# Optimization experiments

Hardware: AMD Instinct MI355X
Metric: run time of the kernel (lower is better)

The kernel has to match this reference:

```python
import jax, jax.numpy as jnp
import numpy as np
import math

HEAD_N = 8
IN_FEATS = 512
BATCH, LENG = 4, 2048
LN_EPS = 1e-5


def setup_inputs() -> dict:
    key = jax.random.key(0)
    ks = jax.random.split(key, 16)
    d = IN_FEATS
    inp = {
        "q": jax.random.normal(ks[0], (BATCH, LENG, d), jnp.float32),
        "k": jax.random.normal(ks[1], (BATCH, LENG, d), jnp.float32),
        "v": jax.random.normal(ks[2], (BATCH, LENG, d), jnp.float32),
        # 4 Linear(in_feats, in_feats): weights [out,in] torch-style, bias [out]
        "Wq": jax.random.normal(ks[3], (d, d), jnp.float32) * 0.02,
        "bq": jnp.zeros((d,), jnp.float32),
        "Wk": jax.random.normal(ks[4], (d, d), jnp.float32) * 0.02,
        "bk": jnp.zeros((d,), jnp.float32),
        "Wv": jax.random.normal(ks[5], (d, d), jnp.float32) * 0.02,
        "bv": jnp.zeros((d,), jnp.float32),
        "Wo": jax.random.normal(ks[6], (d, d), jnp.float32) * 0.02,
        "bo": jnp.zeros((d,), jnp.float32),
        "gamma": jnp.ones((d,), jnp.float32),
        "beta": jnp.zeros((d,), jnp.float32),
    }
    return inp


def _split_heads(x, W, b):
    # Linear then reshape exactly as the torch code: (B,L,D)->(B,L,H,dh)->(B,H,L,dh)->(B*H,L,dh)
    B, L, D = x.shape
    dh = D // HEAD_N
    y = x @ W.T + b
    y = y.reshape(B, L, HEAD_N, dh).transpose(0, 2, 1, 3).reshape(B * HEAD_N, L, dh)
    return y


def reference(q, k, v, Wq, bq, Wk, bk, Wv, bv, Wo, bo, gamma, beta):
    residual = q
    B, L, D = q.shape
    dh = D // HEAD_N
    qh = _split_heads(q, Wq, bq)  # [B*H, L, dh]
    kh = _split_heads(k, Wk, bk)
    vh = _split_heads(v, Wv, bv)

    scores = jnp.einsum("nqd,nkd->nqk", qh, kh) / math.sqrt(dh)  # [B*H, L, L]
    raw_att = jax.nn.softmax(scores, axis=-1)
    att = jnp.einsum("nqk,nkd->nqd", raw_att, vh)  # [B*H, L, dh]

    # Faithful to the original (buggy) merge: reshape (B*H,L,dh) AS IF layout were (H,B,L,dh)
    att = att.reshape(HEAD_N, B, L, dh).transpose(1, 2, 0, 3).reshape(B, L, D)

    att = att @ Wo.T + bo
    # dropout is identity in eval/reference mode
    x = att + residual
    mu = jnp.mean(x, axis=-1, keepdims=True)
    var = jnp.mean(jnp.square(x - mu), axis=-1, keepdims=True)
    out = (x - mu) / jnp.sqrt(var + LN_EPS) * gamma + beta
    return (out, raw_att)
```

## Files before the change

kernel.cpp:

```cpp
#include <hip/hip_runtime.h>
#include <hip/hip_bf16.h>

#define D_MODEL 512
#define SEQ 2048
#define NB 4
#define NH 8
#define DH 64
#define NHEADS 32
#define MROWS 8192

typedef __bf16 bf16_t;
typedef __bf16 bf16x4_t __attribute__((ext_vector_type(4)));
typedef __bf16 bf16x8_t __attribute__((ext_vector_type(8)));
typedef float f32x4_t __attribute__((ext_vector_type(4)));

__device__ inline f32x4_t mfma16(bf16x8_t a, bf16x8_t b, f32x4_t c) {
    return __builtin_amdgcn_mfma_f32_16x16x32_bf16(a, b, c, 0, 0, 0);
}

__global__ __launch_bounds__(256) void qkv_proj_all_kernel(
    const float* __restrict__ qp, const float* __restrict__ kp, const float* __restrict__ vp,
    const float* __restrict__ Wq, const float* __restrict__ bq,
    const float* __restrict__ Wk, const float* __restrict__ bk,
    const float* __restrict__ Wv, const float* __restrict__ bv,
    bf16_t* __restrict__ qfrag, bf16_t* __restrict__ kfrag, bf16_t* __restrict__ vfrag)
{
    __shared__ bf16_t As[128][72];
    __shared__ bf16_t Bs[128][72];

    const int mode = blockIdx.z;
    const float* X    = (mode == 0) ? qp : (mode == 1) ? kp : vp;
    const float* W    = (mode == 0) ? Wq : (mode == 1) ? Wk : Wv;
    const float* bias = (mode == 0) ? bq : (mode == 1) ? bk : bv;
    bf16_t* dst       = (mode == 0) ? qfrag : (mode == 1) ? kfrag : vfrag;

    const int t = threadIdx.x;
    const int lane = t & 63, w = t >> 6;
    const int lr = lane & 15, lg = lane >> 4;
    const int wm = w >> 1, wn = w & 1;
    const int m0 = blockIdx.x * 128, n0 = blockIdx.y * 128;

    f32x4_t acc[4][4];
#pragma unroll
    for (int i = 0; i < 4; i++)
#pragma unroll
        for (int j = 0; j < 4; j++) acc[i][j] = f32x4_t{0.f, 0.f, 0.f, 0.f};

    const int srow = t >> 4;
    const int scol = (t & 15) * 4;

    bf16_t (*Pa)[72] = (mode == 2) ? As : Bs;
    bf16_t (*Pb)[72] = (mode == 2) ? Bs : As;

    for (int kt = 0; kt < 8; kt++) {
        __syncthreads();
#pragma unroll
        for (int p = 0; p < 8; p++) {
            int row = p * 16 + srow;
            float4 va = *(const float4*)(X + (size_t)(m0 + row) * 512 + kt * 64 + scol);
            bf16x4_t ha = { (bf16_t)va.x, (bf16_t)va.y, (bf16_t)va.z, (bf16_t)va.w };
            *(bf16x4_t*)(&As[row][scol]) = ha;
            float4 vb = *(const float4*)(W + (size_t)(n0 + row) * 512 + kt * 64 + scol);
            bf16x4_t hb = { (bf16_t)vb.x, (bf16_t)vb.y, (bf16_t)vb.z, (bf16_t)vb.w };
            *(bf16x4_t*)(&Bs[row][scol]) = hb;
        }
        __syncthreads();
#pragma unroll
        for (int kk = 0; kk < 64; kk += 32) {
            bf16x8_t fa[4], fb[4];
#pragma unroll
            for (int i = 0; i < 4; i++)
                fa[i] = *(const bf16x8_t*)(&Pa[wm * 64 + i * 16 + lr][kk + lg * 8]);
#pragma unroll
            for (int j = 0; j < 4; j++)
                fb[j] = *(const bf16x8_t*)(&Pb[wn * 64 + j * 16 + lr][kk + lg * 8]);
#pragma unroll
            for (int i = 0; i < 4; i++)
#pragma unroll
                for (int j = 0; j < 4; j++)
                    acc[i][j] = mfma16(fa[i], fb[j], acc[i][j]);
        }
    }

    if (mode == 2) {
#pragma unroll
        for (int j = 0; j < 4; j++) {
            int col = n0 + wn * 64 + j * 16 + lr;
            float bval = bias[col];
            int h = col >> 6, d = col & 63;
#pragma unroll
            for (int i = 0; i < 4; i++) {
                int rbase = m0 + wm * 64 + i * 16 + lg * 4;
                int b = rbase >> 11, l0 = rbase & 2047;
                int win = l0 >> 5, kkg = l0 & 31;
                int pos0 = (kkg < 16) ? ((kkg >> 2) * 8) : (((kkg - 16) >> 2) * 8 + 4);
                bf16x4_t hv;
#pragma unroll
                for (int r = 0; r < 4; r++) hv[r] = (bf16_t)(acc[i][j][r] + bval);
                *(bf16x4_t*)(dst + ((((size_t)(b * NH + h) * 64 + win) * 64 + d) * 32 + pos0)) = hv;
            }
        }
    } else {
#pragma unroll
        for (int i = 0; i < 4; i++) {
            int featbase = n0 + wm * 64 + i * 16 + lg * 4;
            float4 b4 = *(const float4*)(bias + featbase);
            float bb[4] = { b4.x, b4.y, b4.z, b4.w };
            int h = featbase >> 6, d0 = featbase & 63;
            int c = (d0 & 31) >> 3, e0 = d0 & 7, fd = (d0 >= 32) ? 1 : 0;
#pragma unroll
            for (int j = 0; j < 4; j++) {
                int seq = m0 + wn * 64 + j * 16 + lr;
                int b = seq >> 11, l = seq & 2047;
                bf16x4_t hv;
#pragma unroll
                for (int r = 0; r < 4; r++) hv[r] = (bf16_t)(acc[i][j][r] + bb[r]);
                size_t idx;
                if (mode == 0) {
                    int qw = l >> 4, lp = (l & 15) + 16 * c;
                    idx = ((((size_t)(b * NH + h) * 128 + qw) * 2 + fd) * 64 + lp) * 8 + e0;
                } else {
                    int win = l >> 5, fk = (((l & 31) >= 16) ? 2 : 0) + fd;
                    int lp = (l & 15) + 16 * c;
                    idx = ((((size_t)(b * NH + h) * 64 + win) * 4 + fk) * 64 + lp) * 8 + e0;
                }
                *(bf16x4_t*)(dst + idx) = hv;
            }
        }
    }
}

__global__ __launch_bounds__(256, 2) void attn_kernel(
    const bf16_t* __restrict__ qfrag, const bf16_t* __restrict__ kfrag,
    const bf16_t* __restrict__ vfrag, float* __restrict__ probs,
    bf16_t* __restrict__ attw)
{
    __shared__ float stage[4][16][132];

    const int bh = blockIdx.y;
    const int t = threadIdx.x;
    const int lane = t & 63, w = t >> 6;
    const int lr = lane & 15, lg = lane >> 4;
    const int q0c0 = blockIdx.x * 128 + w * 32;
    const int q0c1 = q0c0 + 16;
    const int qw0 = q0c0 >> 4;

    const bf16_t* qfb = qfrag + (size_t)bh * 131072;
    const bf16x8_t qA0 = *(const bf16x8_t*)(qfb + ((size_t)(qw0 * 2 + 0) * 64 + lane) * 8);
    const bf16x8_t qA1 = *(const bf16x8_t*)(qfb + ((size_t)(qw0 * 2 + 1) * 64 + lane) * 8);
    const bf16x8_t qB0 = *(const bf16x8_t*)(qfb + ((size_t)(qw0 * 2 + 2) * 64 + lane) * 8);
    const bf16x8_t qB1 = *(const bf16x8_t*)(qfb + ((size_t)(qw0 * 2 + 3) * 64 + lane) * 8);

    const bf16_t* kfb = kfrag + (size_t)bh * 131072;
    const bf16_t* vfb = vfrag + (size_t)bh * 131072;

    float sum0 = 0.f;
    {
        const bf16_t* kp0 = kfb + lane * 8;
        bf16x8_t k00 = *(const bf16x8_t*)(kp0);
        bf16x8_t k01 = *(const bf16x8_t*)(kp0 + 512);
        bf16x8_t k10 = *(const bf16x8_t*)(kp0 + 1024);
        bf16x8_t k11 = *(const bf16x8_t*)(kp0 + 1536);
#pragma unroll 2
        for (int win = 0; win < 64; win++) {
            bf16x8_t n00 = k00, n01 = k01, n10 = k10, n11 = k11;
            if (win < 63) {
                const bf16_t* kp = kfb + (size_t)(win + 1) * 2048 + lane * 8;
                n00 = *(const bf16x8_t*)(kp);
                n01 = *(const bf16x8_t*)(kp + 512);
                n10 = *(const bf16x8_t*)(kp + 1024);
                n11 = *(const bf16x8_t*)(kp + 1536);
            }
            f32x4_t s0 = {0.f, 0.f, 0.f, 0.f}, s1 = {0.f, 0.f, 0.f, 0.f};
            s0 = mfma16(k00, qA0, s0);
            s0 = mfma16(k01, qA1, s0);
            s1 = mfma16(k10, qA0, s1);
            s1 = mfma16(k11, qA1, s1);
#pragma unroll
            for (int r = 0; r < 4; r++)
                sum0 += __expf(s0[r] * 0.125f) + __expf(s1[r] * 0.125f);
            k00 = n00; k01 = n01; k10 = n10; k11 = n11;
        }
    }
    sum0 += __shfl_xor(sum0, 16, 64);
    sum0 += __shfl_xor(sum0, 32, 64);
    const float ri0 = 1.0f / sum0;

    f32x4_t oacc[4];
#pragma unroll
    for (int db = 0; db < 4; db++) oacc[db] = f32x4_t{0.f, 0.f, 0.f, 0.f};
    float sum1 = 0.f;
    {
        float* pb = probs + (size_t)bh * SEQ * SEQ + (size_t)q0c0 * SEQ;
        const bf16_t* kp0 = kfb + lane * 8;
        bf16x8_t k00 = *(const bf16x8_t*)(kp0);
        bf16x8_t k01 = *(const bf16x8_t*)(kp0 + 512);
        bf16x8_t k10 = *(const bf16x8_t*)(kp0 + 1024);
        bf16x8_t k11 = *(const bf16x8_t*)(kp0 + 1536);

        for (int sw = 0; sw < 16; sw++) {
#pragma unroll
            for (int c = 0; c < 4; c++) {
                const int win = sw * 4 + c;
                bf16x8_t av[4];
#pragma unroll
                for (int db = 0; db < 4; db++)
                    av[db] = *(const bf16x8_t*)(vfb + (((size_t)win * 64 + db * 16 + lr) * 32 + lg * 8));
                bf16x8_t n00 = k00, n01 = k01, n10 = k10, n11 = k11;
                if (win < 63) {
                    const bf16_t* kp = kfb + (size_t)(win + 1) * 2048 + lane * 8;
                    n00 = *(const bf16x8_t*)(kp);
                    n01 = *(const bf16x8_t*)(kp + 512);
                    n10 = *(const bf16x8_t*)(kp + 1024);
                    n11 = *(const bf16x8_t*)(kp + 1536);
                }
                f32x4_t s0 = {0.f, 0.f, 0.f, 0.f}, s1 = {0.f, 0.f, 0.f, 0.f};
                s0 = mfma16(k00, qA0, s0);
                s0 = mfma16(k01, qA1, s0);
                s1 = mfma16(k10, qA0, s1);
                s1 = mfma16(k11, qA1, s1);
                float pl[8];
#pragma unroll
                for (int r = 0; r < 4; r++) {
                    pl[r]     = __expf(s0[r] * 0.125f) * ri0;
                    pl[4 + r] = __expf(s1[r] * 0.125f) * ri0;
                }
                const int c0_ = c * 32;
                f32x4_t lo = { pl[0], pl[1], pl[2], pl[3] };
                f32x4_t hi = { pl[4], pl[5], pl[6], pl[7] };
                *(f32x4_t*)(&stage[w][lr][c0_ + lg * 4])      = lo;
                *(f32x4_t*)(&stage[w][lr][c0_ + 16 + lg * 4]) = hi;
                bf16x8_t p;
#pragma unroll
                for (int e = 0; e < 8; e++) p[e] = (bf16_t)pl[e];
#pragma unroll
                for (int db = 0; db < 4; db++)
                    oacc[db] = mfma16(av[db], p, oacc[db]);
                f32x4_t u0 = {0.f, 0.f, 0.f, 0.f}, u1 = {0.f, 0.f, 0.f, 0.f};
                u0 = mfma16(k00, qB0, u0);
                u0 = mfma16(k01, qB1, u0);
                u1 = mfma16(k10, qB0, u1);
                u1 = mfma16(k11, qB1, u1);
#pragma unroll
                for (int r = 0; r < 4; r++)
                    sum1 += __expf(u0[r] * 0.125f) + __expf(u1[r] * 0.125f);
                k00 = n00; k01 = n01; k10 = n10; k11 = n11;
            }
#pragma unroll
            for (int it = 0; it < 8; it++) {
                int row = it * 2 + (lane >> 5);
                int col = (lane & 31) * 4;
                f32x4_t vv = *(const f32x4_t*)(&stage[w][row][col]);
                __builtin_nontemporal_store(vv, (f32x4_t*)(pb + (size_t)row * SEQ + sw * 128 + col));
            }
        }
    }
    sum1 += __shfl_xor(sum1, 16, 64);
    sum1 += __shfl_xor(sum1, 32, 64);
    const float ri1 = 1.0f / sum1;

    {
        float* ow = &stage[w][0][0];
#pragma unroll
        for (int db = 0; db < 4; db++)
#pragma unroll
            for (int r = 0; r < 4; r++)
                ow[(db * 16 + lg * 4 + r) * 17 + lr] = oacc[db][r];
        bf16x8_t h0, h1;
#pragma unroll
        for (int jj = 0; jj < 8; jj++) h0[jj] = (bf16_t)ow[(lg * 16 + jj) * 17 + lr];
#pragma unroll
        for (int jj = 0; jj < 8; jj++) h1[jj] = (bf16_t)ow[(lg * 16 + 8 + jj) * 17 + lr];
        bf16_t* ao = attw + ((size_t)bh * SEQ + q0c0 + lr) * DH + lg * 16;
        *(bf16x8_t*)(ao)     = h0;
        *(bf16x8_t*)(ao + 8) = h1;
    }

#pragma unroll
    for (int db = 0; db < 4; db++) oacc[db] = f32x4_t{0.f, 0.f, 0.f, 0.f};
    {
        float* pb = probs + (size_t)bh * SEQ * SEQ + (size_t)q0c1 * SEQ;
        const bf16_t* kp0 = kfb + lane * 8;
        bf16x8_t k00 = *(const bf16x8_t*)(kp0);
        bf16x8_t k01 = *(const bf16x8_t*)(kp0 + 512);
        bf16x8_t k10 = *(const bf16x8_t*)(kp0 + 1024);
        bf16x8_t k11 = *(const bf16x8_t*)(kp0 + 1536);

        for (int sw = 0; sw < 16; sw++) {
#pragma unroll
            for (int c = 0; c < 4; c++) {
                const int win = sw * 4 + c;
                bf16x8_t av[4];
#pragma unroll
                for (int db = 0; db < 4; db++)
                    av[db] = *(const bf16x8_t*)(vfb + (((size_t)win * 64 + db * 16 + lr) * 32 + lg * 8));
                bf16x8_t n00 = k00, n01 = k01, n10 = k10, n11 = k11;
                if (win < 63) {
                    const bf16_t* kp = kfb + (size_t)(win + 1) * 2048 + lane * 8;
                    n00 = *(const bf16x8_t*)(kp);
                    n01 = *(const bf16x8_t*)(kp + 512);
                    n10 = *(const bf16x8_t*)(kp + 1024);
                    n11 = *(const bf16x8_t*)(kp + 1536);
                }
                f32x4_t s0 = {0.f, 0.f, 0.f, 0.f}, s1 = {0.f, 0.f, 0.f, 0.f};
                s0 = mfma16(k00, qB0, s0);
                s0 = mfma16(k01, qB1, s0);
                s1 = mfma16(k10, qB0, s1);
                s1 = mfma16(k11, qB1, s1);
                float pl[8];
#pragma unroll
                for (int r = 0; r < 4; r++) {
                    pl[r]     = __expf(s0[r] * 0.125f) * ri1;
                    pl[4 + r] = __expf(s1[r] * 0.125f) * ri1;
                }
                const int c0_ = c * 32;
                f32x4_t lo = { pl[0], pl[1], pl[2], pl[3] };
                f32x4_t hi = { pl[4], pl[5], pl[6], pl[7] };
                *(f32x4_t*)(&stage[w][lr][c0_ + lg * 4])      = lo;
                *(f32x4_t*)(&stage[w][lr][c0_ + 16 + lg * 4]) = hi;
                bf16x8_t p;
#pragma unroll
                for (int e = 0; e < 8; e++) p[e] = (bf16_t)pl[e];
#pragma unroll
                for (int db = 0; db < 4; db++)
                    oacc[db] = mfma16(av[db], p, oacc[db]);
                k00 = n00; k01 = n01; k10 = n10; k11 = n11;
            }
#pragma unroll
            for (int it = 0; it < 8; it++) {
                int row = it * 2 + (lane >> 5);
                int col = (lane & 31) * 4;
                f32x4_t vv = *(const f32x4_t*)(&stage[w][row][col]);
                __builtin_nontemporal_store(vv, (f32x4_t*)(pb + (size_t)row * SEQ + sw * 128 + col));
            }
        }
    }

    {
        float* ow = &stage[w][0][0];
#pragma unroll
        for (int db = 0; db < 4; db++)
#pragma unroll
            for (int r = 0; r < 4; r++)
                ow[(db * 16 + lg * 4 + r) * 17 + lr] = oacc[db][r];
        bf16x8_t h0, h1;
#pragma unroll
        for (int jj = 0; jj < 8; jj++) h0[jj] = (bf16_t)ow[(lg * 16 + jj) * 17 + lr];
#pragma unroll
        for (int jj = 0; jj < 8; jj++) h1[jj] = (bf16_t)ow[(lg * 16 + 8 + jj) * 17 + lr];
        bf16_t* ao = attw + ((size_t)bh * SEQ + q0c1 + lr) * DH + lg * 16;
        *(bf16x8_t*)(ao)     = h0;
        *(bf16x8_t*)(ao + 8) = h1;
    }
}

__global__ __launch_bounds__(256) void out_proj_kernel(
    const bf16_t* __restrict__ attw, const float* __restrict__ Wo,
    const float* __restrict__ bo, float* __restrict__ y)
{
    __shared__ bf16_t As[128][72];
    __shared__ bf16_t Bs[128][72];

    const int t = threadIdx.x;
    const int lane = t & 63, w = t >> 6;
    const int lr = lane & 15, lg = lane >> 4;
    const int wm = w >> 1, wn = w & 1;
    const int m0 = blockIdx.x * 128, n0 = blockIdx.y * 128;

    f32x4_t acc[4][4];
#pragma unroll
    for (int i = 0; i < 4; i++)
#pragma unroll
        for (int j = 0; j < 4; j++) acc[i][j] = f32x4_t{0.f, 0.f, 0.f, 0.f};

    const int arow = t >> 3;
    const int acol = (t & 7) * 8;
    const int srow = t >> 4;
    const int scol = (t & 15) * 4;

    for (int kt = 0; kt < 8; kt++) {
        __syncthreads();
#pragma unroll
        for (int p = 0; p < 4; p++) {
            int row = p * 32 + arow;
            int grow = m0 + row;
            int b = grow >> 11, l = grow & 2047;
            bf16x8_t va = *(const bf16x8_t*)(attw + (size_t)((kt * NB + b) * SEQ + l) * DH + acol);
            *(bf16x8_t*)(&As[row][acol]) = va;
        }
#pragma unroll
        for (int p = 0; p < 8; p++) {
            int row = p * 16 + srow;
            float4 vb = *(const float4*)(Wo + (size_t)(n0 + row) * 512 + kt * 64 + scol);
            bf16x4_t hb = { (bf16_t)vb.x, (bf16_t)vb.y, (bf16_t)vb.z, (bf16_t)vb.w };
            *(bf16x4_t*)(&Bs[row][scol]) = hb;
        }
        __syncthreads();
#pragma unroll
        for (int kk = 0; kk < 64; kk += 32) {
            bf16x8_t af[4], bfr[4];
#pragma unroll
            for (int i = 0; i < 4; i++)
                af[i] = *(const bf16x8_t*)(&As[wm * 64 + i * 16 + lr][kk + lg * 8]);
#pragma unroll
            for (int j = 0; j < 4; j++)
                bfr[j] = *(const bf16x8_t*)(&Bs[wn * 64 + j * 16 + lr][kk + lg * 8]);
#pragma unroll
            for (int i = 0; i < 4; i++)
#pragma unroll
                for (int j = 0; j < 4; j++)
                    acc[i][j] = mfma16(af[i], bfr[j], acc[i][j]);
        }
    }

#pragma unroll
    for (int j = 0; j < 4; j++) {
        int col = n0 + wn * 64 + j * 16 + lr;
        float bval = bo[col];
#pragma unroll
        for (int i = 0; i < 4; i++) {
#pragma unroll
            for (int r = 0; r < 4; r++) {
                int row = m0 + wm * 64 + i * 16 + lg * 4 + r;
                y[(size_t)row * 512 + col] = acc[i][j][r] + bval;
            }
        }
    }
}

__global__ __launch_bounds__(256) void ln_kernel(
    const float* __restrict__ y, const float* __restrict__ resid,
    const float* __restrict__ gamma, const float* __restrict__ beta,
    float* __restrict__ out)
{
    const int t = threadIdx.x;
    const int lane = t & 63, w = t >> 6;
    const int row = blockIdx.x * 4 + w;
    const float* yr = y + (size_t)row * 512;
    const float* rr = resid + (size_t)row * 512;
    const int c = lane * 8;

    float4 a0 = *(const float4*)(yr + c);
    float4 a1 = *(const float4*)(yr + c + 4);
    float4 r0 = *(const float4*)(rr + c);
    float4 r1 = *(const float4*)(rr + c + 4);
    float x[8] = { a0.x + r0.x, a0.y + r0.y, a0.z + r0.z, a0.w + r0.w,
                   a1.x + r1.x, a1.y + r1.y, a1.z + r1.z, a1.w + r1.w };

    float s = 0.f, sq = 0.f;
#pragma unroll
    for (int e = 0; e < 8; e++) { s += x[e]; sq += x[e] * x[e]; }
#pragma unroll
    for (int msk = 32; msk >= 1; msk >>= 1) {
        s  += __shfl_xor(s,  msk, 64);
        sq += __shfl_xor(sq, msk, 64);
    }
    float mean = s * (1.f / 512.f);
    float var  = sq * (1.f / 512.f) - mean * mean;
    float rstd = rsqrtf(var + 1e-5f);

    float4 g0 = *(const float4*)(gamma + c);
    float4 g1 = *(const float4*)(gamma + c + 4);
    float4 b0 = *(const float4*)(beta + c);
    float4 b1 = *(const float4*)(beta + c + 4);
    float g[8] = { g0.x, g0.y, g0.z, g0.w, g1.x, g1.y, g1.z, g1.w };
    float bb[8] = { b0.x, b0.y, b0.z, b0.w, b1.x, b1.y, b1.z, b1.w };

    float o[8];
#pragma unroll
    for (int e = 0; e < 8; e++) o[e] = (x[e] - mean) * rstd * g[e] + bb[e];
    float4 o0 = { o[0], o[1], o[2], o[3] };
    float4 o1 = { o[4], o[5], o[6], o[7] };
    float* op = out + (size_t)row * 512 + c;
    *(float4*)(op)     = o0;
    *(float4*)(op + 4) = o1;
}

extern "C" void kernel_launch(void* const* d_in, const int* in_sizes, int n_in,
                              void* d_out, int out_size, void* d_ws, size_t ws_size,
                              hipStream_t stream)
{
    (void)in_sizes; (void)n_in; (void)out_size; (void)ws_size;

    const float* q     = (const float*)d_in[0];
    const float* k     = (const float*)d_in[1];
    const float* v     = (const float*)d_in[2];
    const float* Wq    = (const float*)d_in[3];
    const float* bq    = (const float*)d_in[4];
    const float* Wk    = (const float*)d_in[5];
    const float* bk    = (const float*)d_in[6];
    const float* Wv    = (const float*)d_in[7];
    const float* bv    = (const float*)d_in[8];
    const float* Wo    = (const float*)d_in[9];
    const float* bo    = (const float*)d_in[10];
    const float* gamma = (const float*)d_in[11];
    const float* beta  = (const float*)d_in[12];

    float* out   = (float*)d_out;
    float* probs = out + (size_t)NB * SEQ * D_MODEL;

    char* ws = (char*)d_ws;
    bf16_t* qfrag = (bf16_t*)(ws);
    bf16_t* kfrag = (bf16_t*)(ws + 8388608);
    bf16_t* vfrag = (bf16_t*)(ws + 16777216);
    bf16_t* attw  = (bf16_t*)(ws + 25165824);
    float*  y     = (float*) (ws + 33554432);

    qkv_proj_all_kernel<<<dim3(64, 4, 3), 256, 0, stream>>>(
        q, k, v, Wq, bq, Wk, bk, Wv, bv, qfrag, kfrag, vfrag);
    attn_kernel<<<dim3(16, 32), 256, 0, stream>>>(qfrag, kfrag, vfrag, probs, attw);
    out_proj_kernel<<<dim3(64, 4), 256, 0, stream>>>(attw, Wo, bo, y);
    ln_kernel<<<2048, 256, 0, stream>>>(y, q, gamma, beta, out);
}
```

Baseline: 203.8 us.

## Process four 16-row query chunks per wave with chained sum pipelining

Each wave in the attention kernel now handles 64 query rows as four chained 16-row chunks instead of two. While it writes the probabilities for chunk c, it also computes the softmax denominator for chunk c+1, so the separate denominator pass runs once instead of once per two chunks. The grid shrinks from 512 to 256 blocks, with blockIdx.x swapped to index heads, and launch bounds drop to one block per SIMD-occupancy hint. This cuts the redundant QK^T denominator passes (5/4 passes per chunk instead of 3/2) but leaves fewer blocks than the number of CUs, which may underfill the GPU and reduce latency hiding.

```diff
diff --git a/kernel.cpp b/kernel.cpp
--- a/kernel.cpp
+++ b/kernel.cpp
@@ -130,31 +130,28 @@
     }
 }
 
-__global__ __launch_bounds__(256, 2) void attn_kernel(
+__global__ __launch_bounds__(256, 1) void attn_kernel(
     const bf16_t* __restrict__ qfrag, const bf16_t* __restrict__ kfrag,
     const bf16_t* __restrict__ vfrag, float* __restrict__ probs,
     bf16_t* __restrict__ attw)
 {
     __shared__ float stage[4][16][132];
 
-    const int bh = blockIdx.y;
+    const int bh = blockIdx.x;
     const int t = threadIdx.x;
     const int lane = t & 63, w = t >> 6;
     const int lr = lane & 15, lg = lane >> 4;
-    const int q0c0 = blockIdx.x * 128 + w * 32;
-    const int q0c1 = q0c0 + 16;
-    const int qw0 = q0c0 >> 4;
+    const int qbase = blockIdx.y * 256 + w * 64;
 
     const bf16_t* qfb = qfrag + (size_t)bh * 131072;
-    const bf16x8_t qA0 = *(const bf16x8_t*)(qfb + ((size_t)(qw0 * 2 + 0) * 64 + lane) * 8);
-    const bf16x8_t qA1 = *(const bf16x8_t*)(qfb + ((size_t)(qw0 * 2 + 1) * 64 + lane) * 8);
-    const bf16x8_t qB0 = *(const bf16x8_t*)(qfb + ((size_t)(qw0 * 2 + 2) * 64 + lane) * 8);
-    const bf16x8_t qB1 = *(const bf16x8_t*)(qfb + ((size_t)(qw0 * 2 + 3) * 64 + lane) * 8);
-
     const bf16_t* kfb = kfrag + (size_t)bh * 131072;
     const bf16_t* vfb = vfrag + (size_t)bh * 131072;
 
-    float sum0 = 0.f;
+    int qw = qbase >> 4;
+    bf16x8_t qc0 = *(const bf16x8_t*)(qfb + ((size_t)(qw * 2 + 0) * 64 + lane) * 8);
+    bf16x8_t qc1 = *(const bf16x8_t*)(qfb + ((size_t)(qw * 2 + 1) * 64 + lane) * 8);
+
+    float sum = 0.f;
     {
         const bf16_t* kp0 = kfb + lane * 8;
         bf16x8_t k00 = *(const bf16x8_t*)(kp0);
@@ -172,26 +169,33 @@
                 n11 = *(const bf16x8_t*)(kp + 1536);
             }
             f32x4_t s0 = {0.f, 0.f, 0.f, 0.f}, s1 = {0.f, 0.f, 0.f, 0.f};
-            s0 = mfma16(k00, qA0, s0);
-            s0 = mfma16(k01, qA1, s0);
-            s1 = mfma16(k10, qA0, s1);
-            s1 = mfma16(k11, qA1, s1);
+            s0 = mfma16(k00, qc0, s0);
+            s0 = mfma16(k01, qc1, s0);
+            s1 = mfma16(k10, qc0, s1);
+            s1 = mfma16(k11, qc1, s1);
 #pragma unroll
             for (int r = 0; r < 4; r++)
-                sum0 += __expf(s0[r] * 0.125f) + __expf(s1[r] * 0.125f);
+                sum += __expf(s0[r] * 0.125f) + __expf(s1[r] * 0.125f);
             k00 = n00; k01 = n01; k10 = n10; k11 = n11;
         }
     }
-    sum0 += __shfl_xor(sum0, 16, 64);
-    sum0 += __shfl_xor(sum0, 32, 64);
-    const float ri0 = 1.0f / sum0;
+    sum += __shfl_xor(sum, 16, 64);
+    sum += __shfl_xor(sum, 32, 64);
+    float ri = 1.0f / sum;
 
     f32x4_t oacc[4];
-#pragma unroll
-    for (int db = 0; db < 4; db++) oacc[db] = f32x4_t{0.f, 0.f, 0.f, 0.f};
-    float sum1 = 0.f;
-    {
-        float* pb = probs + (size_t)bh * SEQ * SEQ + (size_t)q0c0 * SEQ;
+
+#pragma unroll 1
+    for (int c = 0; c < 3; c++) {
+        const int q0 = qbase + c * 16;
+        const int qwn = (q0 + 16) >> 4;
+        bf16x8_t qn0 = *(const bf16x8_t*)(qfb + ((size_t)(qwn * 2 + 0) * 64 + lane) * 8);
+        bf16x8_t qn1 = *(const bf16x8_t*)(qfb + ((size_t)(qwn * 2 + 1) * 64 + lane) * 8);
+        float sumN = 0.f;
+#pragma unroll
+        for (int db = 0; db < 4; db++) oacc[db] = f32x4_t{0.f, 0.f, 0.f, 0.f};
+        float* pb = probs + (size_t)bh * SEQ * SEQ + (size_t)q0 * SEQ;
+
         const bf16_t* kp0 = kfb + lane * 8;
         bf16x8_t k00 = *(const bf16x8_t*)(kp0);
         bf16x8_t k01 = *(const bf16x8_t*)(kp0 + 512);
@@ -200,8 +204,8 @@
 
         for (int sw = 0; sw < 16; sw++) {
 #pragma unroll
-            for (int c = 0; c < 4; c++) {
-                const int win = sw * 4 + c;
+            for (int cc = 0; cc < 4; cc++) {
+                const int win = sw * 4 + cc;
                 bf16x8_t av[4];
 #pragma unroll
                 for (int db = 0; db < 4; db++)
@@ -215,17 +219,17 @@
                     n11 = *(const bf16x8_t*)(kp + 1536);
                 }
                 f32x4_t s0 = {0.f, 0.f, 0.f, 0.f}, s1 = {0.f, 0.f, 0.f, 0.f};
-                s0 = mfma16(k00, qA0, s0);
-                s0 = mfma16(k01, qA1, s0);
-                s1 = mfma16(k10, qA0, s1);
-                s1 = mfma16(k11, qA1, s1);
+                s0 = mfma16(k00, qc0, s0);
+                s0 = mfma16(k01, qc1, s0);
+                s1 = mfma16(k10, qc0, s1);
+                s1 = mfma16(k11, qc1, s1);
                 float pl[8];
 #pragma unroll
                 for (int r = 0; r < 4; r++) {
-                    pl[r]     = __expf(s0[r] * 0.125f) * ri0;
-                    pl[4 + r] = __expf(s1[r] * 0.125f) * ri0;
+                    pl[r]     = __expf(s0[r] * 0.125f) * ri;
+                    pl[4 + r] = __expf(s1[r] * 0.125f) * ri;
                 }
-                const int c0_ = c * 32;
+                const int c0_ = cc * 32;
                 f32x4_t lo = { pl[0], pl[1], pl[2], pl[3] };
                 f32x4_t hi = { pl[4], pl[5], pl[6], pl[7] };
                 *(f32x4_t*)(&stage[w][lr][c0_ + lg * 4])      = lo;
@@ -237,13 +241,13 @@
                 for (int db = 0; db < 4; db++)
                     oacc[db] = mfma16(av[db], p, oacc[db]);
                 f32x4_t u0 = {0.f, 0.f, 0.f, 0.f}, u1 = {0.f, 0.f, 0.f, 0.f};
-                u0 = mfma16(k00, qB0, u0);
-                u0 = mfma16(k01, qB1, u0);
-                u1 = mfma16(k10, qB0, u1);
-                u1 = mfma16(k11, qB1, u1);
+                u0 = mfma16(k00, qn0, u0);
+                u0 = mfma16(k01, qn1, u0);
+                u1 = mfma16(k10, qn0, u1);
+                u1 = mfma16(k11, qn1, u1);
 #pragma unroll
                 for (int r = 0; r < 4; r++)
-                    sum1 += __expf(u0[r] * 0.125f) + __expf(u1[r] * 0.125f);
+                    sumN += __expf(u0[r] * 0.125f) + __expf(u1[r] * 0.125f);
                 k00 = n00; k01 = n01; k10 = n10; k11 = n11;
             }
 #pragma unroll
@@ -254,32 +258,36 @@
                 __builtin_nontemporal_store(vv, (f32x4_t*)(pb + (size_t)row * SEQ + sw * 128 + col));
             }
         }
-    }
-    sum1 += __shfl_xor(sum1, 16, 64);
-    sum1 += __shfl_xor(sum1, 32, 64);
-    const float ri1 = 1.0f / sum1;
+
+        {
+            float* ow = &stage[w][0][0];
+#pragma unroll
+            for (int db = 0; db < 4; db++)
+#pragma unroll
+                for (int r = 0; r < 4; r++)
+                    ow[(db * 16 + lg * 4 + r) * 17 + lr] = oacc[db][r];
+            bf16x8_t h0, h1;
+#pragma unroll
+            for (int jj = 0; jj < 8; jj++) h0[jj] = (bf16_t)ow[(lg * 16 + jj) * 17 + lr];
+#pragma unroll
+            for (int jj = 0; jj < 8; jj++) h1[jj] = (bf16_t)ow[(lg * 16 + 8 + jj) * 17 + lr];
+            bf16_t* ao = attw + ((size_t)bh * SEQ + q0 + lr) * DH + lg * 16;
+            *(bf16x8_t*)(ao)     = h0;
+            *(bf16x8_t*)(ao + 8) = h1;
+        }
+
+        sumN += __shfl_xor(sumN, 16, 64);
+        sumN += __shfl_xor(sumN, 32, 64);
+        ri = 1.0f / sumN;
+        qc0 = qn0; qc1 = qn1;
+    }
 
     {
-        float* ow = &stage[w][0][0];
-#pragma unroll
-        for (int db = 0; db < 4; db++)
-#pragma unroll
-            for (int r = 0; r < 4; r++)
-                ow[(db * 16 + lg * 4 + r) * 17 + lr] = oacc[db][r];
-        bf16x8_t h0, h1;
-#pragma unroll
-        for (int jj = 0; jj < 8; jj++) h0[jj] = (bf16_t)ow[(lg * 16 + jj) * 17 + lr];
-#pragma unroll
-        for (int jj = 0; jj < 8; jj++) h1[jj] = (bf16_t)ow[(lg * 16 + 8 + jj) * 17 + lr];
-        bf16_t* ao = attw + ((size_t)bh * SEQ + q0c0 + lr) * DH + lg * 16;
-        *(bf16x8_t*)(ao)     = h0;
-        *(bf16x8_t*)(ao + 8) = h1;
-    }
-
-#pragma unroll
-    for (int db = 0; db < 4; db++) oacc[db] = f32x4_t{0.f, 0.f, 0.f, 0.f};
-    {
-        float* pb = probs + (size_t)bh * SEQ * SEQ + (size_t)q0c1 * SEQ;
+        const int q0 = qbase + 48;
+#pragma unroll
+        for (int db = 0; db < 4; db++) oacc[db] = f32x4_t{0.f, 0.f, 0.f, 0.f};
+        float* pb = probs + (size_t)bh * SEQ * SEQ + (size_t)q0 * SEQ;
+
         const bf16_t* kp0 = kfb + lane * 8;
         bf16x8_t k00 = *(const bf16x8_t*)(kp0);
         bf16x8_t k01 = *(const bf16x8_t*)(kp0 + 512);
@@ -288,8 +296,8 @@
 
         for (int sw = 0; sw < 16; sw++) {
 #pragma unroll
-            for (int c = 0; c < 4; c++) {
-                const int win = sw * 4 + c;
+            for (int cc = 0; cc < 4; cc++) {
+                const int win = sw * 4 + cc;
                 bf16x8_t av[4];
 #pragma unroll
                 for (int db = 0; db < 4; db++)
@@ -303,17 +311,17 @@
                     n11 = *(const bf16x8_t*)(kp + 1536);
                 }
                 f32x4_t s0 = {0.f, 0.f, 0.f, 0.f}, s1 = {0.f, 0.f, 0.f, 0.f};
-                s0 = mfma16(k00, qB0, s0);
-                s0 = mfma16(k01, qB1, s0);
-                s1 = mfma16(k10, qB0, s1);
-                s1 = mfma16(k11, qB1, s1);
+                s0 = mfma16(k00, qc0, s0);
+                s0 = mfma16(k01, qc1, s0);
+                s1 = mfma16(k10, qc0, s1);
+                s1 = mfma16(k11, qc1, s1);
                 float pl[8];
 #pragma unroll
                 for (int r = 0; r < 4; r++) {
-                    pl[r]     = __expf(s0[r] * 0.125f) * ri1;
-                    pl[4 + r] = __expf(s1[r] * 0.125f) * ri1;
+                    pl[r]     = __expf(s0[r] * 0.125f) * ri;
+                    pl[4 + r] = __expf(s1[r] * 0.125f) * ri;
                 }
-                const int c0_ = c * 32;
+                const int c0_ = cc * 32;
                 f32x4_t lo = { pl[0], pl[1], pl[2], pl[3] };
                 f32x4_t hi = { pl[4], pl[5], pl[6], pl[7] };
                 *(f32x4_t*)(&stage[w][lr][c0_ + lg * 4])      = lo;
@@ -334,9 +342,7 @@
                 __builtin_nontemporal_store(vv, (f32x4_t*)(pb + (size_t)row * SEQ + sw * 128 + col));
             }
         }
-    }
-
-    {
+
         float* ow = &stage[w][0][0];
 #pragma unroll
         for (int db = 0; db < 4; db++)
@@ -348,7 +354,7 @@
         for (int jj = 0; jj < 8; jj++) h0[jj] = (bf16_t)ow[(lg * 16 + jj) * 17 + lr];
 #pragma unroll
         for (int jj = 0; jj < 8; jj++) h1[jj] = (bf16_t)ow[(lg * 16 + 8 + jj) * 17 + lr];
-        bf16_t* ao = attw + ((size_t)bh * SEQ + q0c1 + lr) * DH + lg * 16;
+        bf16_t* ao = attw + ((size_t)bh * SEQ + q0 + lr) * DH + lg * 16;
         *(bf16x8_t*)(ao)     = h0;
         *(bf16x8_t*)(ao + 8) = h1;
     }
@@ -508,7 +514,7 @@
 
     qkv_proj_all_kernel<<<dim3(64, 4, 3), 256, 0, stream>>>(
         q, k, v, Wq, bq, Wk, bk, Wv, bv, qfrag, kfrag, vfrag);
-    attn_kernel<<<dim3(16, 32), 256, 0, stream>>>(qfrag, kfrag, vfrag, probs, attw);
+    attn_kernel<<<dim3(32, 8), 256, 0, stream>>>(qfrag, kfrag, vfrag, probs, attw);
     out_proj_kernel<<<dim3(64, 4), 256, 0, stream>>>(attw, Wo, bo, y);
     ln_kernel<<<2048, 256, 0, stream>>>(y, q, gamma, beta, out);
 }
```

After: 229.3 us. 12.5% more time.

## Fuse output projection with residual add and LayerNorm in one kernel

Applied to the files above, without the earlier changes.

Merges the out-projection GEMM and the LayerNorm kernel. Each block now computes full 512-wide rows for 32 output rows, stages the accumulators in shared memory, then adds bias and residual and normalises in place. This removes the fp32 intermediate y round trip through global memory and one kernel launch. In exchange each block re-reads and converts the whole Wo matrix (256 blocks instead of 256 smaller tiles), uses large shared memory (~78KB), and has a small 32-row M tile with lower MFMA reuse.

```diff
diff --git a/kernel.cpp b/kernel.cpp
--- a/kernel.cpp
+++ b/kernel.cpp
@@ -354,126 +354,108 @@
     }
 }
 
-__global__ __launch_bounds__(256) void out_proj_kernel(
+__global__ __launch_bounds__(256, 2) void out_ln_kernel(
     const bf16_t* __restrict__ attw, const float* __restrict__ Wo,
-    const float* __restrict__ bo, float* __restrict__ y)
+    const float* __restrict__ bo, const float* __restrict__ resid,
+    const float* __restrict__ gamma, const float* __restrict__ beta,
+    float* __restrict__ out)
 {
-    __shared__ bf16_t As[128][72];
-    __shared__ bf16_t Bs[128][72];
+    __shared__ __align__(16) char smem[78336];
+    bf16_t (*As)[72] = (bf16_t(*)[72])smem;
+    bf16_t (*Bs)[72] = (bf16_t(*)[72])(smem + 4608);
+    float  (*ow)[516] = (float(*)[516])smem;
 
     const int t = threadIdx.x;
     const int lane = t & 63, w = t >> 6;
     const int lr = lane & 15, lg = lane >> 4;
-    const int wm = w >> 1, wn = w & 1;
-    const int m0 = blockIdx.x * 128, n0 = blockIdx.y * 128;
-
-    f32x4_t acc[4][4];
-#pragma unroll
-    for (int i = 0; i < 4; i++)
-#pragma unroll
-        for (int j = 0; j < 4; j++) acc[i][j] = f32x4_t{0.f, 0.f, 0.f, 0.f};
-
-    const int arow = t >> 3;
-    const int acol = (t & 7) * 8;
-    const int srow = t >> 4;
-    const int scol = (t & 15) * 4;
+    const int wr = w >> 1, wc = w & 1;
+    const int m0 = blockIdx.x * 32;
+
+    f32x4_t acc[16];
+#pragma unroll
+    for (int j = 0; j < 16; j++) acc[j] = f32x4_t{0.f, 0.f, 0.f, 0.f};
 
     for (int kt = 0; kt < 8; kt++) {
         __syncthreads();
-#pragma unroll
-        for (int p = 0; p < 4; p++) {
-            int row = p * 32 + arow;
+        {
+            int row = t >> 3, d0 = (t & 7) * 8;
             int grow = m0 + row;
             int b = grow >> 11, l = grow & 2047;
-            bf16x8_t va = *(const bf16x8_t*)(attw + (size_t)((kt * NB + b) * SEQ + l) * DH + acol);
-            *(bf16x8_t*)(&As[row][acol]) = va;
+            bf16x8_t va = *(const bf16x8_t*)(attw + (size_t)((kt * NB + b) * SEQ + l) * DH + d0);
+            *(bf16x8_t*)(&As[row][d0]) = va;
         }
 #pragma unroll
         for (int p = 0; p < 8; p++) {
-            int row = p * 16 + srow;
-            float4 vb = *(const float4*)(Wo + (size_t)(n0 + row) * 512 + kt * 64 + scol);
-            bf16x4_t hb = { (bf16_t)vb.x, (bf16_t)vb.y, (bf16_t)vb.z, (bf16_t)vb.w };
-            *(bf16x4_t*)(&Bs[row][scol]) = hb;
+            int row = p * 64 + (t >> 2);
+            int c0 = (t & 3) * 16;
+            const float* wp = Wo + (size_t)row * 512 + kt * 64 + c0;
+#pragma unroll
+            for (int it = 0; it < 4; it++) {
+                float4 v4 = *(const float4*)(wp + it * 4);
+                bf16x4_t hb = { (bf16_t)v4.x, (bf16_t)v4.y, (bf16_t)v4.z, (bf16_t)v4.w };
+                *(bf16x4_t*)(&Bs[row][c0 + it * 4]) = hb;
+            }
         }
         __syncthreads();
 #pragma unroll
         for (int kk = 0; kk < 64; kk += 32) {
-            bf16x8_t af[4], bfr[4];
-#pragma unroll
-            for (int i = 0; i < 4; i++)
-                af[i] = *(const bf16x8_t*)(&As[wm * 64 + i * 16 + lr][kk + lg * 8]);
-#pragma unroll
-            for (int j = 0; j < 4; j++)
-                bfr[j] = *(const bf16x8_t*)(&Bs[wn * 64 + j * 16 + lr][kk + lg * 8]);
-#pragma unroll
-            for (int i = 0; i < 4; i++)
-#pragma unroll
-                for (int j = 0; j < 4; j++)
-                    acc[i][j] = mfma16(af[i], bfr[j], acc[i][j]);
-        }
-    }
-
-#pragma unroll
-    for (int j = 0; j < 4; j++) {
-        int col = n0 + wn * 64 + j * 16 + lr;
-        float bval = bo[col];
-#pragma unroll
-        for (int i = 0; i < 4; i++) {
-#pragma unroll
-            for (int r = 0; r < 4; r++) {
-                int row = m0 + wm * 64 + i * 16 + lg * 4 + r;
-                y[(size_t)row * 512 + col] = acc[i][j][r] + bval;
-            }
-        }
-    }
-}
-
-__global__ __launch_bounds__(256) void ln_kernel(
-    const float* __restrict__ y, const float* __restrict__ resid,
-    const float* __restrict__ gamma, const float* __restrict__ beta,
-    float* __restrict__ out)
-{
-    const int t = threadIdx.x;
-    const int lane = t & 63, w = t >> 6;
-    const int row = blockIdx.x * 4 + w;
-    const float* yr = y + (size_t)row * 512;
-    const float* rr = resid + (size_t)row * 512;
-    const int c = lane * 8;
-
-    float4 a0 = *(const float4*)(yr + c);
-    float4 a1 = *(const float4*)(yr + c + 4);
-    float4 r0 = *(const float4*)(rr + c);
-    float4 r1 = *(const float4*)(rr + c + 4);
-    float x[8] = { a0.x + r0.x, a0.y + r0.y, a0.z + r0.z, a0.w + r0.w,
-                   a1.x + r1.x, a1.y + r1.y, a1.z + r1.z, a1.w + r1.w };
-
-    float s = 0.f, sq = 0.f;
-#pragma unroll
-    for (int e = 0; e < 8; e++) { s += x[e]; sq += x[e] * x[e]; }
-#pragma unroll
-    for (int msk = 32; msk >= 1; msk >>= 1) {
-        s  += __shfl_xor(s,  msk, 64);
-        sq += __shfl_xor(sq, msk, 64);
-    }
-    float mean = s * (1.f / 512.f);
-    float var  = sq * (1.f / 512.f) - mean * mean;
-    float rstd = rsqrtf(var + 1e-5f);
-
-    float4 g0 = *(const float4*)(gamma + c);
-    float4 g1 = *(const float4*)(gamma + c + 4);
-    float4 b0 = *(const float4*)(beta + c);
-    float4 b1 = *(const float4*)(beta + c + 4);
-    float g[8] = { g0.x, g0.y, g0.z, g0.w, g1.x, g1.y, g1.z, g1.w };
-    float bb[8] = { b0.x, b0.y, b0.z, b0.w, b1.x, b1.y, b1.z, b1.w };
-
-    float o[8];
-#pragma unroll
-    for (int e = 0; e < 8; e++) o[e] = (x[e] - mean) * rstd * g[e] + bb[e];
-    float4 o0 = { o[0], o[1], o[2], o[3] };
-    float4 o1 = { o[4], o[5], o[6], o[7] };
-    float* op = out + (size_t)row * 512 + c;
-    *(float4*)(op)     = o0;
-    *(float4*)(op + 4) = o1;
+            bf16x8_t af = *(const bf16x8_t*)(&As[wr * 16 + lr][kk + lg * 8]);
+#pragma unroll
+            for (int j = 0; j < 16; j++) {
+                bf16x8_t bfr = *(const bf16x8_t*)(&Bs[wc * 256 + j * 16 + lr][kk + lg * 8]);
+                acc[j] = mfma16(af, bfr, acc[j]);
+            }
+        }
+    }
+
+    __syncthreads();
+#pragma unroll
+    for (int j = 0; j < 16; j++)
+#pragma unroll
+        for (int r = 0; r < 4; r++)
+            ow[wr * 16 + lg * 4 + r][wc * 256 + j * 16 + lr] = acc[j][r];
+    __syncthreads();
+
+    const int hrow = lane >> 5;
+    const int c0 = (lane & 31) * 4;
+#pragma unroll
+    for (int rp = 0; rp < 4; rp++) {
+        int row = w * 8 + rp * 2 + hrow;
+        int grow = m0 + row;
+        const float* rr = resid + (size_t)grow * 512;
+        f32x4_t x[4];
+        float s = 0.f, sq = 0.f;
+#pragma unroll
+        for (int it = 0; it < 4; it++) {
+            f32x4_t oy = *(const f32x4_t*)(&ow[row][c0 + it * 128]);
+            f32x4_t bb = *(const f32x4_t*)(bo + c0 + it * 128);
+            f32x4_t qv = *(const f32x4_t*)(rr + c0 + it * 128);
+            f32x4_t xv = { oy[0] + bb[0] + qv[0], oy[1] + bb[1] + qv[1],
+                           oy[2] + bb[2] + qv[2], oy[3] + bb[3] + qv[3] };
+            x[it] = xv;
+#pragma unroll
+            for (int e = 0; e < 4; e++) { s += xv[e]; sq += xv[e] * xv[e]; }
+        }
+#pragma unroll
+        for (int msk = 16; msk >= 1; msk >>= 1) {
+            s  += __shfl_xor(s,  msk, 64);
+            sq += __shfl_xor(sq, msk, 64);
+        }
+        float mean = s * (1.f / 512.f);
+        float var  = sq * (1.f / 512.f) - mean * mean;
+        float rstd = rsqrtf(var + 1e-5f);
+        float* op = out + (size_t)grow * 512;
+#pragma unroll
+        for (int it = 0; it < 4; it++) {
+            f32x4_t gv = *(const f32x4_t*)(gamma + c0 + it * 128);
+            f32x4_t bv = *(const f32x4_t*)(beta + c0 + it * 128);
+            f32x4_t ov;
+#pragma unroll
+            for (int e = 0; e < 4; e++)
+                ov[e] = (x[it][e] - mean) * rstd * gv[e] + bv[e];
+            *(f32x4_t*)(op + c0 + it * 128) = ov;
+        }
+    }
 }
 
 extern "C" void kernel_launch(void* const* d_in, const int* in_sizes, int n_in,
@@ -504,11 +486,9 @@
     bf16_t* kfrag = (bf16_t*)(ws + 8388608);
     bf16_t* vfrag = (bf16_t*)(ws + 16777216);
     bf16_t* attw  = (bf16_t*)(ws + 25165824);
-    float*  y     = (float*) (ws + 33554432);
 
     qkv_proj_all_kernel<<<dim3(64, 4, 3), 256, 0, stream>>>(
         q, k, v, Wq, bq, Wk, bk, Wv, bv, qfrag, kfrag, vfrag);
     attn_kernel<<<dim3(16, 32), 256, 0, stream>>>(qfrag, kfrag, vfrag, probs, attw);
-    out_proj_kernel<<<dim3(64, 4), 256, 0, stream>>>(attw, Wo, bo, y);
-    ln_kernel<<<2048, 256, 0, stream>>>(y, q, gamma, beta, out);
+    out_ln_kernel<<<256, 256, 0, stream>>>(attw, Wo, bo, q, gamma, beta, out);
 }
```

New measurement: 212.0 us. 1.04x slower.
